# Kernel optimization log

Hardware: AMD Instinct MI355X
Metric: run time of the kernel (lower is better)

Reference implementation:

```python
import jax, jax.numpy as jnp
import numpy as np

N = 100000
E = 1600000
F_IN = 256
H1, C1 = 8, 8
NUM_CLASSES = 40
NEG_SLOPE = 0.2


def setup_inputs() -> dict:
    key = jax.random.key(0)
    ks = jax.random.split(key, 12)
    x = jax.random.normal(ks[0], (N, F_IN), dtype=jnp.float32)
    ei = jax.random.randint(ks[1], (2, E), 0, N, dtype=jnp.int64)
    # PyG GATConv default add_self_loops=True
    loops = jnp.stack([jnp.arange(N, dtype=jnp.int64)] * 2)
    edge_index = jnp.concatenate([ei, loops], axis=1)  # [2, E+N]
    s1 = 1.0 / np.sqrt(F_IN)
    s2 = 1.0 / np.sqrt(H1 * C1)
    W1 = jax.random.normal(ks[2], (F_IN, H1 * C1), dtype=jnp.float32) * s1
    att_src1 = jax.random.normal(ks[3], (H1, C1), dtype=jnp.float32) * 0.1
    att_dst1 = jax.random.normal(ks[4], (H1, C1), dtype=jnp.float32) * 0.1
    b1 = jnp.zeros((H1 * C1,), dtype=jnp.float32)
    W2 = jax.random.normal(ks[5], (H1 * C1, NUM_CLASSES), dtype=jnp.float32) * s2
    att_src2 = jax.random.normal(ks[6], (1, NUM_CLASSES), dtype=jnp.float32) * 0.1
    att_dst2 = jax.random.normal(ks[7], (1, NUM_CLASSES), dtype=jnp.float32) * 0.1
    b2 = jnp.zeros((NUM_CLASSES,), dtype=jnp.float32)
    return {"x": x, "W1": W1, "att_src1": att_src1, "att_dst1": att_dst1,
            "b1": b1, "W2": W2, "att_src2": att_src2, "att_dst2": att_dst2,
            "b2": b2, "edge_index": edge_index}


def gat_layer(x, W, a_src, a_dst, b, src, dst, heads, out_ch, concat):
    n = x.shape[0]
    h = (x @ W).reshape(n, heads, out_ch)              # [N,H,C]
    alpha_src = (h * a_src[None]).sum(-1)              # [N,H]
    alpha_dst = (h * a_dst[None]).sum(-1)              # [N,H]
    e = jax.nn.leaky_relu(alpha_src[src] + alpha_dst[dst], NEG_SLOPE)  # [E,H]
    m = jax.ops.segment_max(e, dst, num_segments=n)    # per-dst softmax (stable)
    e = jnp.exp(e - m[dst])
    denom = jax.ops.segment_sum(e, dst, num_segments=n)
    w = e / denom[dst]                                 # [E,H]
    msg = h[src] * w[:, :, None]                       # [E,H,C]
    out = jax.ops.segment_sum(msg, dst, num_segments=n)  # [N,H,C]
    out = out.reshape(n, heads * out_ch) if concat else out.mean(axis=1)
    return out + b


def reference(x, W1, att_src1, att_dst1, b1, W2, att_src2, att_dst2, b2, edge_index):
    src, dst = edge_index[0], edge_index[1]
    h = gat_layer(x, W1, att_src1, att_dst1, b1, src, dst, H1, C1, concat=True)
    h = jax.nn.elu(h)
    out = gat_layer(h, W2, att_src2, att_dst2, b2, src, dst, 1, NUM_CLASSES, concat=False)
    return jax.nn.log_softmax(out, axis=1)
```

## Files before the change

kernel.cpp:

```cpp
#include <hip/hip_runtime.h>
#include <hip/hip_bf16.h>

#define NEG_SLOPE 0.2f

typedef __attribute__((ext_vector_type(8))) short short8;
typedef __attribute__((ext_vector_type(4))) float f32x4;

__device__ __forceinline__ float lrelu(float x) { return x >= 0.f ? x : NEG_SLOPE * x; }

__device__ __forceinline__ unsigned pack_bf2(float a, float b) {
    unsigned ua = __float_as_uint(a), ub = __float_as_uint(b);
    ua = (ua + 0x7fffu + ((ua >> 16) & 1u)) >> 16;
    ub = (ub + 0x7fffu + ((ub >> 16) & 1u)) & 0xffff0000u;
    return ua | ub;
}
__device__ __forceinline__ float2 unpack_bf2(unsigned u) {
    return make_float2(__uint_as_float(u << 16), __uint_as_float(u & 0xffff0000u));
}
__device__ __forceinline__ unsigned short bf16_of(float a) {
    unsigned ua = __float_as_uint(a);
    return (unsigned short)((ua + 0x7fffu + ((ua >> 16) & 1u)) >> 16);
}

#define NBLK 256

__global__ __launch_bounds__(256) void pcount_kernel(const int* __restrict__ dst,
                                                     int* __restrict__ blk_cnt,
                                                     int etot, int npart, int chunk) {
    __shared__ int cnt[800];
    for (int c = threadIdx.x; c < npart; c += 256) cnt[c] = 0;
    __syncthreads();
    int e0 = blockIdx.x * chunk, e1 = min(etot, e0 + chunk);
    for (int e = e0 + (int)threadIdx.x; e < e1; e += 256)
        atomicAdd(&cnt[dst[e] >> 7], 1);
    __syncthreads();
    for (int c = threadIdx.x; c < npart; c += 256)
        blk_cnt[(size_t)blockIdx.x * npart + c] = cnt[c];
}

__global__ __launch_bounds__(256) void pscanA_kernel(const int* __restrict__ blk_cnt,
                                                     int* __restrict__ blk_base,
                                                     int* __restrict__ ptot, int npart) {
    __shared__ int sm[256];
    int t = threadIdx.x, c = blockIdx.x;
    int v = blk_cnt[(size_t)t * npart + c];
    sm[t] = v;
    __syncthreads();
    for (int off = 1; off < 256; off <<= 1) {
        int u = (t >= off) ? sm[t - off] : 0;
        __syncthreads();
        sm[t] += u;
        __syncthreads();
    }
    blk_base[(size_t)t * npart + c] = sm[t] - v;
    if (t == 255) ptot[c] = sm[t];
}

__global__ __launch_bounds__(1024) void pscanB_kernel(const int* __restrict__ ptot,
                                                      int* __restrict__ colbase,
                                                      int npart, int etot) {
    __shared__ int sm[1024];
    int t = threadIdx.x;
    int v = (t < npart) ? ptot[t] : 0;
    sm[t] = v;
    __syncthreads();
    for (int off = 1; off < 1024; off <<= 1) {
        int u = (t >= off) ? sm[t - off] : 0;
        __syncthreads();
        sm[t] += u;
        __syncthreads();
    }
    if (t < npart) colbase[t] = sm[t] - v;
    if (t == 0) colbase[npart] = etot;
}

__global__ __launch_bounds__(256) void pscatter_kernel(const int* __restrict__ src,
                                                       const int* __restrict__ dst,
                                                       const int* __restrict__ blk_base,
                                                       const int* __restrict__ colbase,
                                                       int2* __restrict__ eb,
                                                       int etot, int npart, int chunk) {
    __shared__ int cur[800];
    for (int c = threadIdx.x; c < npart; c += 256)
        cur[c] = colbase[c] + blk_base[(size_t)blockIdx.x * npart + c];
    __syncthreads();
    int e0 = blockIdx.x * chunk, e1 = min(etot, e0 + chunk);
    for (int e = e0 + (int)threadIdx.x; e < e1; e += 256) {
        int d = dst[e], s = src[e];
        int pos = atomicAdd(&cur[d >> 7], 1);
        eb[pos] = make_int2(d, s);
    }
}

__global__ __launch_bounds__(256) void build_kernel(const int2* __restrict__ eb,
                                                    const int* __restrict__ colbase,
                                                    int* __restrict__ row_ptr,
                                                    int* __restrict__ csr_src,
                                                    int n, int etot) {
    __shared__ int cnt[128];
    __shared__ int sm[128];
    __shared__ int cur[128];
    int p = blockIdx.x, t = threadIdx.x;
    int lo = p << 7;
    int e0 = colbase[p], e1 = colbase[p + 1];
    if (t < 128) cnt[t] = 0;
    __syncthreads();
    for (int e = e0 + t; e < e1; e += 256)
        atomicAdd(&cnt[eb[e].x & 127], 1);
    __syncthreads();
    int v = 0;
    if (t < 128) { v = cnt[t]; sm[t] = v; }
    __syncthreads();
    for (int off = 1; off < 128; off <<= 1) {
        int u = (t < 128 && t >= off) ? sm[t - off] : 0;
        __syncthreads();
        if (t < 128) sm[t] += u;
        __syncthreads();
    }
    if (t < 128) {
        int ex = e0 + sm[t] - v;
        cur[t] = ex;
        int node = lo + t;
        if (node < n) row_ptr[node] = ex;
    }
    if (p == 0 && t == 0) row_ptr[n] = etot;
    __syncthreads();
    for (int e = e0 + t; e < e1; e += 256) {
        int2 ds = eb[e];
        int pos = atomicAdd(&cur[ds.x & 127], 1);
        csr_src[pos] = ds.y;
    }
}

__global__ __launch_bounds__(256) void w1cvt_kernel(const float* __restrict__ W1,
                                                    unsigned short* __restrict__ W1t) {
    int t = blockIdx.x * 256 + threadIdx.x;
    int k = t >> 6, nn = t & 63;
    W1t[(size_t)nn * 256 + k] = bf16_of(W1[t]);
}

__global__ __launch_bounds__(256) void gemm1_kernel(const float* __restrict__ x,
                                                    const unsigned short* __restrict__ W1t,
                                                    unsigned short* __restrict__ h1b, int n) {
    int tid = threadIdx.x;
    int w = tid >> 6, lane = tid & 63;
    int p = lane & 15, quad = lane >> 4;
    int r0 = blockIdx.x * 64;
    int row = r0 + 16 * w + p;
    const float* xrow = x + (size_t)row * 256;
    f32x4 z = {0.f, 0.f, 0.f, 0.f};
    f32x4 acc[4] = {z, z, z, z};
#pragma unroll
    for (int kc = 0; kc < 8; ++kc) {
        int k0 = kc * 32 + quad * 8;
        float4 v0 = make_float4(0.f, 0.f, 0.f, 0.f), v1 = v0;
        if (row < n) {
            v0 = *(const float4*)(xrow + k0);
            v1 = *(const float4*)(xrow + k0 + 4);
        }
        union { uint4 u; short8 s; } a;
        a.u = make_uint4(pack_bf2(v0.x, v0.y), pack_bf2(v0.z, v0.w),
                         pack_bf2(v1.x, v1.y), pack_bf2(v1.z, v1.w));
#pragma unroll
        for (int t = 0; t < 4; ++t) {
            short8 b = *(const short8*)(W1t + (size_t)(16 * t + p) * 256 + k0);
            acc[t] = __builtin_amdgcn_mfma_f32_16x16x32_bf16(a.s, b, acc[t], 0, 0, 0);
        }
    }
#pragma unroll
    for (int t = 0; t < 4; ++t)
#pragma unroll
        for (int r = 0; r < 4; ++r) {
            int gr = r0 + 16 * w + quad * 4 + r;
            if (gr < n) h1b[(size_t)gr * 64 + 16 * t + p] = bf16_of(acc[t][r]);
        }
}

__global__ __launch_bounds__(256) void alpha1_kernel(const unsigned short* __restrict__ h1b,
                                                     const float* __restrict__ att_s,
                                                     const float* __restrict__ att_d,
                                                     float* __restrict__ as1,
                                                     float* __restrict__ ad1, int n) {
    int wid = threadIdx.x >> 6, lane = threadIdx.x & 63;
    int p = lane & 31;
    int r = blockIdx.x * 8 + wid * 2 + (lane >> 5);
    if (r >= n) return;
    float2 sc = *(const float2*)(att_s + 2 * p);
    float2 dc = *(const float2*)(att_d + 2 * p);
    float2 h = unpack_bf2(((const unsigned*)h1b)[(size_t)r * 32 + p]);
    float ps = h.x * sc.x + h.y * sc.y;
    float pd = h.x * dc.x + h.y * dc.y;
    ps += __shfl_xor(ps, 1); pd += __shfl_xor(pd, 1);
    ps += __shfl_xor(ps, 2); pd += __shfl_xor(pd, 2);
    if ((p & 3) == 0) {
        as1[(size_t)r * 8 + (p >> 2)] = ps;
        ad1[(size_t)r * 8 + (p >> 2)] = pd;
    }
}

__global__ __launch_bounds__(256) void agg1_kernel(const unsigned short* __restrict__ h1b,
                                                   const float* __restrict__ as1,
                                                   const float* __restrict__ ad1,
                                                   const float* __restrict__ b1,
                                                   const int* __restrict__ row_ptr,
                                                   const int* __restrict__ csr_src,
                                                   float* __restrict__ elu1, int n) {
    int lane = threadIdx.x & 63;
    int node = blockIdx.x * 4 + (threadIdx.x >> 6);
    if (node >= n) return;
    int start = row_ptr[node], end = row_ptr[node + 1];
    int slot = lane >> 3, hd = lane & 7;
    float adh = ad1[(size_t)node * 8 + hd];
    int q = lane >> 5, p = lane & 31, hp = p >> 2;
    const unsigned* h1u = (const unsigned*)h1b;
    float2 o = make_float2(0.f, 0.f);
    float den = 0.f;
    for (int base = start; base < end; base += 64) {
        int nloc = min(64, end - base);
        int eidx = base + lane;
        int sAll = (eidx < end) ? csr_src[eidx] : 0;
        for (int e0 = 0; e0 < nloc; e0 += 8) {
            int s = __shfl(sAll, e0 + slot);
            float v = lrelu(as1[(size_t)s * 8 + hd] + adh);
            float w = (e0 + slot < nloc) ? __expf(v) : 0.f;
            den += w;
#pragma unroll
            for (int j = 0; j < 8; j += 2) {
                int sj = __shfl(s, (j + q) * 8);
                float wj = __shfl(w, (j + q) * 8 + hp);
                float2 hf = unpack_bf2(h1u[(size_t)sj * 32 + p]);
                o.x = fmaf(hf.x, wj, o.x);
                o.y = fmaf(hf.y, wj, o.y);
            }
        }
    }
    den += __shfl_xor(den, 8);
    den += __shfl_xor(den, 16);
    den += __shfl_xor(den, 32);
    float inv = 1.f / __shfl(den, hp);
    o.x += __shfl_xor(o.x, 32);
    o.y += __shfl_xor(o.y, 32);
    if (lane < 32) {
        float2 bb = *(const float2*)(b1 + 2 * p);
        float v0 = o.x * inv + bb.x, v1 = o.y * inv + bb.y;
        v0 = v0 > 0.f ? v0 : __expf(v0) - 1.f;
        v1 = v1 > 0.f ? v1 : __expf(v1) - 1.f;
        *(float2*)(elu1 + (size_t)node * 64 + 2 * p) = make_float2(v0, v1);
    }
}

__global__ __launch_bounds__(256) void gemm2_kernel(const float* __restrict__ elu1,
                                                    const float* __restrict__ W2,
                                                    const float* __restrict__ att_s,
                                                    const float* __restrict__ att_d,
                                                    unsigned short* __restrict__ h2b,
                                                    float* __restrict__ as2,
                                                    float* __restrict__ ad2, int n) {
    __shared__ float As[64][132];
    __shared__ float Bs[64][40];
    int tid = threadIdx.x;
    int r0 = blockIdx.x * 128;
    int cx = tid & 7, ry = tid >> 3;
    float sa[5], da[5];
#pragma unroll
    for (int j = 0; j < 5; ++j) {
        sa[j] = att_s[5 * cx + j];
        da[j] = att_d[5 * cx + j];
    }
    for (int t = tid; t < 640; t += 256) {
        int k = t / 10, cq = t % 10;
        *(float4*)&Bs[k][4 * cq] = *(const float4*)(W2 + (size_t)k * 40 + 4 * cq);
    }
    for (int t = tid; t < 2048; t += 256) {
        int row = t >> 4, kq = t & 15;
        int gr = r0 + row;
        float4 av = make_float4(0.f, 0.f, 0.f, 0.f);
        if (gr < n) av = *(const float4*)(elu1 + (size_t)gr * 64 + 4 * kq);
        As[4 * kq + 0][row] = av.x;
        As[4 * kq + 1][row] = av.y;
        As[4 * kq + 2][row] = av.z;
        As[4 * kq + 3][row] = av.w;
    }
    __syncthreads();
    float acc[4][5] = {{0.f}};
#pragma unroll 8
    for (int k = 0; k < 64; ++k) {
        float4 a = *(const float4*)&As[k][4 * ry];
        float ar[4] = {a.x, a.y, a.z, a.w};
        float br[5];
#pragma unroll
        for (int j = 0; j < 5; ++j) br[j] = Bs[k][5 * cx + j];
#pragma unroll
        for (int i = 0; i < 4; ++i)
#pragma unroll
            for (int j = 0; j < 5; ++j) acc[i][j] = fmaf(ar[i], br[j], acc[i][j]);
    }
#pragma unroll
    for (int i = 0; i < 4; ++i) {
        int gr = r0 + 4 * ry + i;
        float ps = 0.f, pd = 0.f;
#pragma unroll
        for (int j = 0; j < 5; ++j) {
            ps = fmaf(acc[i][j], sa[j], ps);
            pd = fmaf(acc[i][j], da[j], pd);
        }
        ps += __shfl_xor(ps, 1); pd += __shfl_xor(pd, 1);
        ps += __shfl_xor(ps, 2); pd += __shfl_xor(pd, 2);
        ps += __shfl_xor(ps, 4); pd += __shfl_xor(pd, 4);
        if (gr < n) {
#pragma unroll
            for (int j = 0; j < 5; ++j) h2b[(size_t)gr * 40 + 5 * cx + j] = bf16_of(acc[i][j]);
            if (cx == 0) {
                as2[gr] = ps;
                ad2[gr] = pd;
            }
        }
    }
}

__global__ __launch_bounds__(256) void agg2_kernel(const unsigned short* __restrict__ h2b,
                                                   const float* __restrict__ as2,
                                                   const float* __restrict__ ad2,
                                                   const float* __restrict__ b2,
                                                   const int* __restrict__ row_ptr,
                                                   const int* __restrict__ csr_src,
                                                   float* __restrict__ out, int n) {
    int lane = threadIdx.x & 63;
    int node = blockIdx.x * 4 + (threadIdx.x >> 6);
    if (node >= n) return;
    int start = row_ptr[node], end = row_ptr[node + 1];
    float adn = ad2[node];

    int q = lane >> 5, p = lane & 31;
    int pc = min(p, 19);
    const unsigned* h2u = (const unsigned*)h2b;
    float2 o = make_float2(0.f, 0.f);
    float den = 0.f;
    for (int base = start; base < end; base += 64) {
        int nloc = min(64, end - base);
        int eidx = base + lane;
        bool valid = eidx < end;
        int sAll = valid ? csr_src[eidx] : 0;
        float v = lrelu(as2[sAll] + adn);
        float w = valid ? __expf(v) : 0.f;
        den += w;
        for (int g = 0; g < nloc; g += 8) {
#pragma unroll
            for (int j = 0; j < 8; j += 2) {
                int idx = g + j + q;
                int sj = __shfl(sAll, idx);
                float wj = __shfl(w, idx);
                float2 hf = unpack_bf2(h2u[(size_t)sj * 20 + pc]);
                o.x = fmaf(hf.x, wj, o.x);
                o.y = fmaf(hf.y, wj, o.y);
            }
        }
    }
#pragma unroll
    for (int off = 1; off < 64; off <<= 1) den += __shfl_xor(den, off);
    float inv = 1.f / den;
    o.x += __shfl_xor(o.x, 32);
    o.y += __shfl_xor(o.y, 32);
    bool act = (lane < 32) && (p < 20);
    float v0 = -1e30f, v1 = -1e30f;
    if (act) {
        float2 bb = *(const float2*)(b2 + 2 * p);
        v0 = o.x * inv + bb.x;
        v1 = o.y * inv + bb.y;
    }
    float vm = fmaxf(v0, v1);
#pragma unroll
    for (int off = 1; off < 64; off <<= 1) vm = fmaxf(vm, __shfl_xor(vm, off));
    float ex = act ? (__expf(v0 - vm) + __expf(v1 - vm)) : 0.f;
#pragma unroll
    for (int off = 1; off < 64; off <<= 1) ex += __shfl_xor(ex, off);
    if (act) {
        float lg = __logf(ex);
        *(float2*)(out + (size_t)node * 40 + 2 * p) = make_float2(v0 - vm - lg, v1 - vm - lg);
    }
}

extern "C" void kernel_launch(void* const* d_in, const int* in_sizes, int n_in,
                              void* d_out, int out_size, void* d_ws, size_t ws_size,
                              hipStream_t stream) {
    const float* x        = (const float*)d_in[0];
    const float* W1       = (const float*)d_in[1];
    const float* att_src1 = (const float*)d_in[2];
    const float* att_dst1 = (const float*)d_in[3];
    const float* b1       = (const float*)d_in[4];
    const float* W2       = (const float*)d_in[5];
    const float* att_src2 = (const float*)d_in[6];
    const float* att_dst2 = (const float*)d_in[7];
    const float* b2       = (const float*)d_in[8];
    const int*   ei       = (const int*)d_in[9];

    int n    = in_sizes[0] / 256;
    int etot = in_sizes[9] / 2;
    const int* srcp = ei;
    const int* dstp = ei + etot;

    int npart = (n + 127) >> 7;
    int chunk = (etot + NBLK - 1) / NBLK;

    char* ws = (char*)d_ws;
    size_t off = 0;
    unsigned short* h1b = (unsigned short*)(ws + off); off += (size_t)n * 64 * 2;
    unsigned short* h2b = (unsigned short*)(ws + off); off += (size_t)n * 40 * 2;
    unsigned short* W1t = (unsigned short*)(ws + off); off += (size_t)64 * 256 * 2;
    float* elu1 = (float*)(ws + off); off += (size_t)n * 64 * 4;
    float* as1  = (float*)(ws + off); off += (size_t)n * 8 * 4;
    float* ad1  = (float*)(ws + off); off += (size_t)n * 8 * 4;
    float* as2  = (float*)(ws + off); off += (size_t)n * 4;
    float* ad2  = (float*)(ws + off); off += (size_t)n * 4;
    int* row_ptr = (int*)(ws + off); off += (size_t)(n + 64) * 4;
    int* csr_src = (int*)(ws + off); off += (size_t)etot * 4;
    int* blk_cnt = (int*)(ws + off); off += (size_t)NBLK * npart * 4;
    int* blk_base= (int*)(ws + off); off += (size_t)NBLK * npart * 4;
    int* ptot    = (int*)(ws + off); off += (size_t)npart * 4;
    int* colbase = (int*)(ws + off); off += (size_t)(npart + 1) * 4;
    float* outp = (float*)d_out;

    int2* eb = (int2*)elu1;

    pcount_kernel<<<NBLK, 256, 0, stream>>>(dstp, blk_cnt, etot, npart, chunk);
    pscanA_kernel<<<npart, 256, 0, stream>>>(blk_cnt, blk_base, ptot, npart);
    pscanB_kernel<<<1, 1024, 0, stream>>>(ptot, colbase, npart, etot);
    pscatter_kernel<<<NBLK, 256, 0, stream>>>(srcp, dstp, blk_base, colbase, eb, etot, npart, chunk);
    build_kernel<<<npart, 256, 0, stream>>>(eb, colbase, row_ptr, csr_src, n, etot);

    int nb4 = (n + 3) / 4;
    w1cvt_kernel<<<64, 256, 0, stream>>>(W1, W1t);
    gemm1_kernel<<<(n + 63) / 64, 256, 0, stream>>>(x, W1t, h1b, n);
    alpha1_kernel<<<(n + 7) / 8, 256, 0, stream>>>(h1b, att_src1, att_dst1, as1, ad1, n);
    agg1_kernel<<<nb4, 256, 0, stream>>>(h1b, as1, ad1, b1, row_ptr, csr_src, elu1, n);
    gemm2_kernel<<<(n + 127) / 128, 256, 0, stream>>>(elu1, W2, att_src2, att_dst2, h2b, as2, ad2, n);
    agg2_kernel<<<nb4, 256, 0, stream>>>(h2b, as2, ad2, b2, row_ptr, csr_src, outp, n);
}
```

Baseline: 388.1 us.

## Co-launch GEMM1/alpha with CSR partition passes, pack edge buffer, use packed FMA

Merges gemm1 with the partition count pass, and alpha1 with the per-partition scan, into combined launches that pick their role by block index. Independent work can then overlap and fewer kernels are launched. The edge bucket buffer now packs dst-low-bits and src into one int instead of an int2, halving scatter and build traffic. The aggregation loops split full 8-edge groups from the tail and use v_pk_fma_f32 through inline asm. Packing assumes src fits in 25 bits, which holds for N=100000.

```diff
diff --git a/kernel.cpp b/kernel.cpp
--- a/kernel.cpp
+++ b/kernel.cpp
@@ -5,6 +5,7 @@
 
 typedef __attribute__((ext_vector_type(8))) short short8;
 typedef __attribute__((ext_vector_type(4))) float f32x4;
+typedef __attribute__((ext_vector_type(2))) float f32x2;
 
 __device__ __forceinline__ float lrelu(float x) { return x >= 0.f ? x : NEG_SLOPE * x; }
 
@@ -17,43 +18,129 @@
 __device__ __forceinline__ float2 unpack_bf2(unsigned u) {
     return make_float2(__uint_as_float(u << 16), __uint_as_float(u & 0xffff0000u));
 }
+__device__ __forceinline__ f32x2 unpack_bf2v(unsigned u) {
+    f32x2 r;
+    r.x = __uint_as_float(u << 16);
+    r.y = __uint_as_float(u & 0xffff0000u);
+    return r;
+}
 __device__ __forceinline__ unsigned short bf16_of(float a) {
     unsigned ua = __float_as_uint(a);
     return (unsigned short)((ua + 0x7fffu + ((ua >> 16) & 1u)) >> 16);
 }
+__device__ __forceinline__ f32x2 pk_fma(f32x2 a, f32x2 b, f32x2 c) {
+    asm("v_pk_fma_f32 %0, %1, %2, %0" : "+v"(c) : "v"(a), "v"(b));
+    return c;
+}
 
 #define NBLK 256
 
-__global__ __launch_bounds__(256) void pcount_kernel(const int* __restrict__ dst,
+__device__ __forceinline__ void gemm1_body(int bid, const float* __restrict__ x,
+                                           const unsigned short* __restrict__ W1t,
+                                           unsigned short* __restrict__ h1b, int n) {
+    int tid = threadIdx.x;
+    int w = tid >> 6, lane = tid & 63;
+    int p = lane & 15, quad = lane >> 4;
+    int r0 = bid * 64;
+    int row = r0 + 16 * w + p;
+    const float* xrow = x + (size_t)row * 256;
+    f32x4 z = {0.f, 0.f, 0.f, 0.f};
+    f32x4 acc[4] = {z, z, z, z};
+#pragma unroll
+    for (int kc = 0; kc < 8; ++kc) {
+        int k0 = kc * 32 + quad * 8;
+        float4 v0 = make_float4(0.f, 0.f, 0.f, 0.f), v1 = v0;
+        if (row < n) {
+            v0 = *(const float4*)(xrow + k0);
+            v1 = *(const float4*)(xrow + k0 + 4);
+        }
+        union { uint4 u; short8 s; } a;
+        a.u = make_uint4(pack_bf2(v0.x, v0.y), pack_bf2(v0.z, v0.w),
+                         pack_bf2(v1.x, v1.y), pack_bf2(v1.z, v1.w));
+#pragma unroll
+        for (int t = 0; t < 4; ++t) {
+            short8 b = *(const short8*)(W1t + (size_t)(16 * t + p) * 256 + k0);
+            acc[t] = __builtin_amdgcn_mfma_f32_16x16x32_bf16(a.s, b, acc[t], 0, 0, 0);
+        }
+    }
+#pragma unroll
+    for (int t = 0; t < 4; ++t)
+#pragma unroll
+        for (int r = 0; r < 4; ++r) {
+            int gr = r0 + 16 * w + quad * 4 + r;
+            if (gr < n) h1b[(size_t)gr * 64 + 16 * t + p] = bf16_of(acc[t][r]);
+        }
+}
+
+__global__ __launch_bounds__(256) void fusedA_kernel(const float* __restrict__ x,
+                                                     const unsigned short* __restrict__ W1t,
+                                                     unsigned short* __restrict__ h1b, int n,
+                                                     const int* __restrict__ dst,
                                                      int* __restrict__ blk_cnt,
-                                                     int etot, int npart, int chunk) {
-    __shared__ int cnt[800];
-    for (int c = threadIdx.x; c < npart; c += 256) cnt[c] = 0;
-    __syncthreads();
-    int e0 = blockIdx.x * chunk, e1 = min(etot, e0 + chunk);
-    for (int e = e0 + (int)threadIdx.x; e < e1; e += 256)
-        atomicAdd(&cnt[dst[e] >> 7], 1);
-    __syncthreads();
-    for (int c = threadIdx.x; c < npart; c += 256)
-        blk_cnt[(size_t)blockIdx.x * npart + c] = cnt[c];
-}
-
-__global__ __launch_bounds__(256) void pscanA_kernel(const int* __restrict__ blk_cnt,
+                                                     int etot, int npart, int chunk, int g1) {
+    if ((int)blockIdx.x < g1) {
+        gemm1_body(blockIdx.x, x, W1t, h1b, n);
+    } else {
+        __shared__ int cnt[800];
+        int bid = blockIdx.x - g1;
+        for (int c = threadIdx.x; c < npart; c += 256) cnt[c] = 0;
+        __syncthreads();
+        int e0 = bid * chunk, e1 = min(etot, e0 + chunk);
+        for (int e = e0 + (int)threadIdx.x; e < e1; e += 256)
+            atomicAdd(&cnt[dst[e] >> 7], 1);
+        __syncthreads();
+        for (int c = threadIdx.x; c < npart; c += 256)
+            blk_cnt[(size_t)bid * npart + c] = cnt[c];
+    }
+}
+
+__device__ __forceinline__ void alpha1_body(int bid, const unsigned short* __restrict__ h1b,
+                                            const float* __restrict__ att_s,
+                                            const float* __restrict__ att_d,
+                                            float* __restrict__ as1,
+                                            float* __restrict__ ad1, int n) {
+    int wid = threadIdx.x >> 6, lane = threadIdx.x & 63;
+    int p = lane & 31;
+    int r = bid * 8 + wid * 2 + (lane >> 5);
+    if (r >= n) return;
+    float2 sc = *(const float2*)(att_s + 2 * p);
+    float2 dc = *(const float2*)(att_d + 2 * p);
+    float2 h = unpack_bf2(((const unsigned*)h1b)[(size_t)r * 32 + p]);
+    float ps = h.x * sc.x + h.y * sc.y;
+    float pd = h.x * dc.x + h.y * dc.y;
+    ps += __shfl_xor(ps, 1); pd += __shfl_xor(pd, 1);
+    ps += __shfl_xor(ps, 2); pd += __shfl_xor(pd, 2);
+    if ((p & 3) == 0) {
+        as1[(size_t)r * 8 + (p >> 2)] = ps;
+        ad1[(size_t)r * 8 + (p >> 2)] = pd;
+    }
+}
+
+__global__ __launch_bounds__(256) void fusedB_kernel(const unsigned short* __restrict__ h1b,
+                                                     const float* __restrict__ att_s,
+                                                     const float* __restrict__ att_d,
+                                                     float* __restrict__ as1,
+                                                     float* __restrict__ ad1, int n,
+                                                     const int* __restrict__ blk_cnt,
                                                      int* __restrict__ blk_base,
-                                                     int* __restrict__ ptot, int npart) {
-    __shared__ int sm[256];
-    int t = threadIdx.x, c = blockIdx.x;
-    int v = blk_cnt[(size_t)t * npart + c];
-    sm[t] = v;
-    __syncthreads();
-    for (int off = 1; off < 256; off <<= 1) {
-        int u = (t >= off) ? sm[t - off] : 0;
-        __syncthreads();
-        sm[t] += u;
-        __syncthreads();
-    }
-    blk_base[(size_t)t * npart + c] = sm[t] - v;
-    if (t == 255) ptot[c] = sm[t];
+                                                     int* __restrict__ ptot, int npart, int ga) {
+    if ((int)blockIdx.x < ga) {
+        alpha1_body(blockIdx.x, h1b, att_s, att_d, as1, ad1, n);
+    } else {
+        __shared__ int sm[256];
+        int t = threadIdx.x, c = blockIdx.x - ga;
+        int v = blk_cnt[(size_t)t * npart + c];
+        sm[t] = v;
+        __syncthreads();
+        for (int off = 1; off < 256; off <<= 1) {
+            int u = (t >= off) ? sm[t - off] : 0;
+            __syncthreads();
+            sm[t] += u;
+            __syncthreads();
+        }
+        blk_base[(size_t)t * npart + c] = sm[t] - v;
+        if (t == 255) ptot[c] = sm[t];
+    }
 }
 
 __global__ __launch_bounds__(1024) void pscanB_kernel(const int* __restrict__ ptot,
@@ -78,7 +165,7 @@
                                                        const int* __restrict__ dst,
                                                        const int* __restrict__ blk_base,
                                                        const int* __restrict__ colbase,
-                                                       int2* __restrict__ eb,
+                                                       int* __restrict__ eb,
                                                        int etot, int npart, int chunk) {
     __shared__ int cur[800];
     for (int c = threadIdx.x; c < npart; c += 256)
@@ -88,11 +175,11 @@
     for (int e = e0 + (int)threadIdx.x; e < e1; e += 256) {
         int d = dst[e], s = src[e];
         int pos = atomicAdd(&cur[d >> 7], 1);
-        eb[pos] = make_int2(d, s);
-    }
-}
-
-__global__ __launch_bounds__(256) void build_kernel(const int2* __restrict__ eb,
+        eb[pos] = (d & 127) | (s << 7);
+    }
+}
+
+__global__ __launch_bounds__(256) void build_kernel(const int* __restrict__ eb,
                                                     const int* __restrict__ colbase,
                                                     int* __restrict__ row_ptr,
                                                     int* __restrict__ csr_src,
@@ -106,7 +193,7 @@
     if (t < 128) cnt[t] = 0;
     __syncthreads();
     for (int e = e0 + t; e < e1; e += 256)
-        atomicAdd(&cnt[eb[e].x & 127], 1);
+        atomicAdd(&cnt[eb[e] & 127], 1);
     __syncthreads();
     int v = 0;
     if (t < 128) { v = cnt[t]; sm[t] = v; }
@@ -126,9 +213,9 @@
     if (p == 0 && t == 0) row_ptr[n] = etot;
     __syncthreads();
     for (int e = e0 + t; e < e1; e += 256) {
-        int2 ds = eb[e];
-        int pos = atomicAdd(&cur[ds.x & 127], 1);
-        csr_src[pos] = ds.y;
+        int u = eb[e];
+        int pos = atomicAdd(&cur[u & 127], 1);
+        csr_src[pos] = u >> 7;
     }
 }
 
@@ -137,65 +224,6 @@
     int t = blockIdx.x * 256 + threadIdx.x;
     int k = t >> 6, nn = t & 63;
     W1t[(size_t)nn * 256 + k] = bf16_of(W1[t]);
-}
-
-__global__ __launch_bounds__(256) void gemm1_kernel(const float* __restrict__ x,
-                                                    const unsigned short* __restrict__ W1t,
-                                                    unsigned short* __restrict__ h1b, int n) {
-    int tid = threadIdx.x;
-    int w = tid >> 6, lane = tid & 63;
-    int p = lane & 15, quad = lane >> 4;
-    int r0 = blockIdx.x * 64;
-    int row = r0 + 16 * w + p;
-    const float* xrow = x + (size_t)row * 256;
-    f32x4 z = {0.f, 0.f, 0.f, 0.f};
-    f32x4 acc[4] = {z, z, z, z};
-#pragma unroll
-    for (int kc = 0; kc < 8; ++kc) {
-        int k0 = kc * 32 + quad * 8;
-        float4 v0 = make_float4(0.f, 0.f, 0.f, 0.f), v1 = v0;
-        if (row < n) {
-            v0 = *(const float4*)(xrow + k0);
-            v1 = *(const float4*)(xrow + k0 + 4);
-        }
-        union { uint4 u; short8 s; } a;
-        a.u = make_uint4(pack_bf2(v0.x, v0.y), pack_bf2(v0.z, v0.w),
-                         pack_bf2(v1.x, v1.y), pack_bf2(v1.z, v1.w));
-#pragma unroll
-        for (int t = 0; t < 4; ++t) {
-            short8 b = *(const short8*)(W1t + (size_t)(16 * t + p) * 256 + k0);
-            acc[t] = __builtin_amdgcn_mfma_f32_16x16x32_bf16(a.s, b, acc[t], 0, 0, 0);
-        }
-    }
-#pragma unroll
-    for (int t = 0; t < 4; ++t)
-#pragma unroll
-        for (int r = 0; r < 4; ++r) {
-            int gr = r0 + 16 * w + quad * 4 + r;
-            if (gr < n) h1b[(size_t)gr * 64 + 16 * t + p] = bf16_of(acc[t][r]);
-        }
-}
-
-__global__ __launch_bounds__(256) void alpha1_kernel(const unsigned short* __restrict__ h1b,
-                                                     const float* __restrict__ att_s,
-                                                     const float* __restrict__ att_d,
-                                                     float* __restrict__ as1,
-                                                     float* __restrict__ ad1, int n) {
-    int wid = threadIdx.x >> 6, lane = threadIdx.x & 63;
-    int p = lane & 31;
-    int r = blockIdx.x * 8 + wid * 2 + (lane >> 5);
-    if (r >= n) return;
-    float2 sc = *(const float2*)(att_s + 2 * p);
-    float2 dc = *(const float2*)(att_d + 2 * p);
-    float2 h = unpack_bf2(((const unsigned*)h1b)[(size_t)r * 32 + p]);
-    float ps = h.x * sc.x + h.y * sc.y;
-    float pd = h.x * dc.x + h.y * dc.y;
-    ps += __shfl_xor(ps, 1); pd += __shfl_xor(pd, 1);
-    ps += __shfl_xor(ps, 2); pd += __shfl_xor(pd, 2);
-    if ((p & 3) == 0) {
-        as1[(size_t)r * 8 + (p >> 2)] = ps;
-        ad1[(size_t)r * 8 + (p >> 2)] = pd;
-    }
 }
 
 __global__ __launch_bounds__(256) void agg1_kernel(const unsigned short* __restrict__ h1b,
@@ -213,24 +241,37 @@
     float adh = ad1[(size_t)node * 8 + hd];
     int q = lane >> 5, p = lane & 31, hp = p >> 2;
     const unsigned* h1u = (const unsigned*)h1b;
-    float2 o = make_float2(0.f, 0.f);
+    f32x2 o = {0.f, 0.f};
     float den = 0.f;
     for (int base = start; base < end; base += 64) {
         int nloc = min(64, end - base);
         int eidx = base + lane;
         int sAll = (eidx < end) ? csr_src[eidx] : 0;
-        for (int e0 = 0; e0 < nloc; e0 += 8) {
+        int e0 = 0;
+        for (; e0 + 8 <= nloc; e0 += 8) {
+            int s = __shfl(sAll, e0 + slot);
+            float v = lrelu(as1[(size_t)s * 8 + hd] + adh);
+            float w = __expf(v);
+            den += w;
+#pragma unroll
+            for (int j = 0; j < 8; j += 2) {
+                int sj = __shfl(s, (j + q) * 8);
+                float wj = __shfl(w, (j + q) * 8 + hp);
+                f32x2 w2 = {wj, wj};
+                o = pk_fma(unpack_bf2v(h1u[(size_t)sj * 32 + p]), w2, o);
+            }
+        }
+        if (e0 < nloc) {
             int s = __shfl(sAll, e0 + slot);
             float v = lrelu(as1[(size_t)s * 8 + hd] + adh);
             float w = (e0 + slot < nloc) ? __expf(v) : 0.f;
             den += w;
-#pragma unroll
-            for (int j = 0; j < 8; j += 2) {
+            int jmax = nloc - e0;
+            for (int j = 0; j < jmax; j += 2) {
                 int sj = __shfl(s, (j + q) * 8);
                 float wj = __shfl(w, (j + q) * 8 + hp);
-                float2 hf = unpack_bf2(h1u[(size_t)sj * 32 + p]);
-                o.x = fmaf(hf.x, wj, o.x);
-                o.y = fmaf(hf.y, wj, o.y);
+                f32x2 w2 = {wj, wj};
+                o = pk_fma(unpack_bf2v(h1u[(size_t)sj * 32 + p]), w2, o);
             }
         }
     }
@@ -334,7 +375,7 @@
     int q = lane >> 5, p = lane & 31;
     int pc = min(p, 19);
     const unsigned* h2u = (const unsigned*)h2b;
-    float2 o = make_float2(0.f, 0.f);
+    f32x2 o = {0.f, 0.f};
     float den = 0.f;
     for (int base = start; base < end; base += 64) {
         int nloc = min(64, end - base);
@@ -344,15 +385,25 @@
         float v = lrelu(as2[sAll] + adn);
         float w = valid ? __expf(v) : 0.f;
         den += w;
-        for (int g = 0; g < nloc; g += 8) {
+        int g = 0;
+        for (; g + 8 <= nloc; g += 8) {
 #pragma unroll
             for (int j = 0; j < 8; j += 2) {
                 int idx = g + j + q;
                 int sj = __shfl(sAll, idx);
                 float wj = __shfl(w, idx);
-                float2 hf = unpack_bf2(h2u[(size_t)sj * 20 + pc]);
-                o.x = fmaf(hf.x, wj, o.x);
-                o.y = fmaf(hf.y, wj, o.y);
+                f32x2 w2 = {wj, wj};
+                o = pk_fma(unpack_bf2v(h2u[(size_t)sj * 20 + pc]), w2, o);
+            }
+        }
+        if (g < nloc) {
+            int jmax = nloc - g;
+            for (int j = 0; j < jmax; j += 2) {
+                int idx = g + j + q;
+                int sj = __shfl(sAll, idx);
+                float wj = __shfl(w, idx);
+                f32x2 w2 = {wj, wj};
+                o = pk_fma(unpack_bf2v(h2u[(size_t)sj * 20 + pc]), w2, o);
             }
         }
     }
@@ -420,18 +471,19 @@
     int* colbase = (int*)(ws + off); off += (size_t)(npart + 1) * 4;
     float* outp = (float*)d_out;
 
-    int2* eb = (int2*)elu1;
-
-    pcount_kernel<<<NBLK, 256, 0, stream>>>(dstp, blk_cnt, etot, npart, chunk);
-    pscanA_kernel<<<npart, 256, 0, stream>>>(blk_cnt, blk_base, ptot, npart);
+    int* eb = (int*)elu1;
+
+    int g1 = (n + 63) / 64;
+    int ga = (n + 7) / 8;
+    int nb4 = (n + 3) / 4;
+
+    w1cvt_kernel<<<64, 256, 0, stream>>>(W1, W1t);
+    fusedA_kernel<<<g1 + NBLK, 256, 0, stream>>>(x, W1t, h1b, n, dstp, blk_cnt, etot, npart, chunk, g1);
+    fusedB_kernel<<<ga + npart, 256, 0, stream>>>(h1b, att_src1, att_dst1, as1, ad1, n,
+                                                  blk_cnt, blk_base, ptot, npart, ga);
     pscanB_kernel<<<1, 1024, 0, stream>>>(ptot, colbase, npart, etot);
     pscatter_kernel<<<NBLK, 256, 0, stream>>>(srcp, dstp, blk_base, colbase, eb, etot, npart, chunk);
     build_kernel<<<npart, 256, 0, stream>>>(eb, colbase, row_ptr, csr_src, n, etot);
-
-    int nb4 = (n + 3) / 4;
-    w1cvt_kernel<<<64, 256, 0, stream>>>(W1, W1t);
-    gemm1_kernel<<<(n + 63) / 64, 256, 0, stream>>>(x, W1t, h1b, n);
-    alpha1_kernel<<<(n + 7) / 8, 256, 0, stream>>>(h1b, att_src1, att_dst1, as1, ad1, n);
     agg1_kernel<<<nb4, 256, 0, stream>>>(h1b, as1, ad1, b1, row_ptr, csr_src, elu1, n);
     gemm2_kernel<<<(n + 127) / 128, 256, 0, stream>>>(elu1, W2, att_src2, att_dst2, h2b, as2, ad2, n);
     agg2_kernel<<<nb4, 256, 0, stream>>>(h2b, as2, ad2, b2, row_ptr, csr_src, outp, n);
```

Result: no change. 386.4 us (-0.4%).
